# Kernel optimization log

Measured on AMD Instinct MI355X. Metric: run time of the kernel, lower is better.

The kernel has to match this reference:

```python
import jax, jax.numpy as jnp
import numpy as np

N_NODES = 50000
N_EDGES = 800000
IN_CH = 128
EDGE_DIM = 32
H1, H2, H3, OUT = 128, 64, 32, 1


def _linear_params(key, fan_in, fan_out, bias=True):
    k1, k2 = jax.random.split(key)
    scale = 1.0 / np.sqrt(fan_in)
    W = jax.random.uniform(k1, (fan_in, fan_out), jnp.float32, -scale, scale)
    if bias:
        b = jax.random.uniform(k2, (fan_out,), jnp.float32, -scale, scale)
        return W, b
    return W


def setup_inputs() -> dict:
    key = jax.random.key(0)
    ks = jax.random.split(key, 32)
    inp = {
        'x': jax.random.normal(ks[0], (N_NODES, IN_CH), jnp.float32),
        'edge_index': jax.random.randint(ks[1], (2, N_EDGES), 0, N_NODES, jnp.int64),
        'edge_attr': jax.random.normal(ks[2], (N_EDGES, EDGE_DIM), jnp.float32),
    }
    dims = [(IN_CH, H1), (H1, H2), (H2, H3)]
    ki = 3
    for l, (fi, fo) in enumerate(dims, start=1):
        inp[f'Wq{l}'], inp[f'bq{l}'] = _linear_params(ks[ki], fi, fo); ki += 1
        inp[f'Wk{l}'], inp[f'bk{l}'] = _linear_params(ks[ki], fi, fo); ki += 1
        inp[f'Wv{l}'], inp[f'bv{l}'] = _linear_params(ks[ki], fi, fo); ki += 1
        inp[f'We{l}'] = _linear_params(ks[ki], EDGE_DIM, fo, bias=False); ki += 1
        inp[f'Ws{l}'], inp[f'bs{l}'] = _linear_params(ks[ki], fi, fo); ki += 1
    inp['Wc'], inp['bc'] = _linear_params(ks[ki], H3, OUT)
    return inp


def _tconv(x, src, dst, edge_attr, Wq, bq, Wk, bk, Wv, bv, We, Ws, bs):
    # TransformerConv, heads=1: edge-conditioned attention with segment softmax over dst
    q = x @ Wq + bq                      # [N, d]
    k = x @ Wk + bk                      # [N, d]
    v = x @ Wv + bv                      # [N, d]
    e = edge_attr @ We                   # [E, d]
    k_e = k[src] + e                     # gather + edge key
    v_e = v[src] + e                     # gather + edge value
    d = q.shape[-1]
    alpha = jnp.sum(q[dst] * k_e, axis=-1) / jnp.sqrt(jnp.asarray(d, x.dtype))  # [E]
    m = jax.ops.segment_max(alpha, dst, num_segments=N_NODES)
    a = jnp.exp(alpha - m[dst])
    s = jax.ops.segment_sum(a, dst, num_segments=N_NODES)
    a = a / s[dst]
    agg = jax.ops.segment_sum(a[:, None] * v_e, dst, num_segments=N_NODES)
    return agg + x @ Ws + bs             # root/skip connection


def reference(x, edge_index, edge_attr,
              Wq1, bq1, Wk1, bk1, Wv1, bv1, We1, Ws1, bs1,
              Wq2, bq2, Wk2, bk2, Wv2, bv2, We2, Ws2, bs2,
              Wq3, bq3, Wk3, bk3, Wv3, bv3, We3, Ws3, bs3,
              Wc, bc):
    src, dst = edge_index[0], edge_index[1]
    h = jax.nn.relu(_tconv(x, src, dst, edge_attr, Wq1, bq1, Wk1, bk1, Wv1, bv1, We1, Ws1, bs1))
    h = jax.nn.relu(_tconv(h, src, dst, edge_attr, Wq2, bq2, Wk2, bk2, Wv2, bv2, We2, Ws2, bs2))
    h = jax.nn.relu(_tconv(h, src, dst, edge_attr, Wq3, bq3, Wk3, bk3, Wv3, bv3, We3, Ws3, bs3))
    return h @ Wc + bc
```

## Files before the change

kernel.cpp:

```cpp
#include <hip/hip_runtime.h>
#include <math.h>

#define N_NODES 50000
#define N_EDGES 800000

typedef __bf16 bf16;
typedef __bf16 bf16x8 __attribute__((ext_vector_type(8)));
typedef float f32x4 __attribute__((ext_vector_type(4)));

__device__ __forceinline__ float bflo(unsigned r) {
  union { unsigned u; float f; } c; c.u = r << 16; return c.f;
}
__device__ __forceinline__ float bfhi(unsigned r) {
  union { unsigned u; float f; } c; c.u = r & 0xffff0000u; return c.f;
}

__device__ __forceinline__ float dot2bf(unsigned a, unsigned b, float acc) {
#if defined(__has_builtin)
#if __has_builtin(__builtin_amdgcn_fdot2_f32_bf16)
  typedef __bf16 bf16x2 __attribute__((ext_vector_type(2)));
  union { unsigned u; bf16x2 v; } ca, cb;
  ca.u = a; cb.u = b;
  return __builtin_amdgcn_fdot2_f32_bf16(ca.v, cb.v, acc, false);
#else
  return acc + bflo(a) * bflo(b) + bfhi(a) * bfhi(b);
#endif
#else
  return acc + bflo(a) * bflo(b) + bfhi(a) * bfhi(b);
#endif
}

__global__ void k_detect(const int* ei, int* flags) {
  if (threadIdx.x == 0 && blockIdx.x == 0) {
    int is64 = 1;
    for (int i = 0; i < 128; ++i) {
      if (ei[2 * i + 1] != 0) { is64 = 0; break; }
    }
    flags[0] = is64;
  }
}

__device__ __forceinline__ int load_idx(const int* ei, int e, int is64, int which) {
  size_t idx = (size_t)which * N_EDGES + (size_t)e;
  return is64 ? ei[2 * idx] : ei[idx];
}


__global__ void k_zero(int* p, int n) {
  int i = blockIdx.x * blockDim.x + threadIdx.x;
  if (i < n) p[i] = 0;
}

__global__ void k_hist(const int* ei, const int* flags, int* counts) {
  int e = blockIdx.x * blockDim.x + threadIdx.x;
  int is64 = flags[0];
  if (e < N_EDGES) {
    int dst = load_idx(ei, e, is64, 1);
    if (dst >= 0 && dst < N_NODES) atomicAdd(&counts[dst], 1);
  }
}

__global__ void k_scan1(const int* counts, int* row_ptr, int* bsum) {
  __shared__ int buf[1024];
  int t = threadIdx.x;
  int i = blockIdx.x * 1024 + t;
  int v = (i < N_NODES) ? counts[i] : 0;
  buf[t] = v;
  __syncthreads();
  for (int off = 1; off < 1024; off <<= 1) {
    int x = (t >= off) ? buf[t - off] : 0;
    __syncthreads();
    buf[t] += x;
    __syncthreads();
  }
  if (i < N_NODES) row_ptr[i] = buf[t] - v;
  if (t == 1023) bsum[blockIdx.x] = buf[1023];
}

__global__ void k_scan2(int* bsum, int* row_ptr) {
  constexpr int NB = (N_NODES + 1023) / 1024;
  int t = threadIdx.x;
  int v = (t < NB) ? bsum[t] : 0;
  int inc = v;
#pragma unroll
  for (int off = 1; off < 64; off <<= 1) {
    int x = __shfl_up(inc, off, 64);
    if (t >= off) inc += x;
  }
  if (t < NB) bsum[t] = inc - v;
  if (t == 63) row_ptr[N_NODES] = inc;
}

__global__ void k_scan3(const int* bsum, int* row_ptr, int* cursor) {
  int i = blockIdx.x * 1024 + threadIdx.x;
  if (i < N_NODES) {
    int r = row_ptr[i] + bsum[blockIdx.x];
    row_ptr[i] = r;
    cursor[i] = r;
  }
}

__global__ void k_scatter(const int* ei, const int* flags, int* cursor,
                          int* csr_src, int* csr_eid) {
  int e = blockIdx.x * blockDim.x + threadIdx.x;
  int is64 = flags[0];
  if (e < N_EDGES) {
    int src = load_idx(ei, e, is64, 0);
    int dst = load_idx(ei, e, is64, 1);
    if (dst >= 0 && dst < N_NODES && src >= 0 && src < N_NODES) {
      int pos = atomicAdd(&cursor[dst], 1);
      if (pos >= 0 && pos < N_EDGES) {
        csr_src[pos] = src;
        csr_eid[pos] = e;
      }
    }
  }
}


__global__ void k_eaperm(const float* __restrict__ ea, const int* __restrict__ csr_eid,
                         bf16* __restrict__ ea_bf) {
  int idx = blockIdx.x * blockDim.x + threadIdx.x;
  if (idx >= N_EDGES * 16) return;
  int p = idx >> 4, jj = idx & 15;
  int eid = csr_eid[p];
  float2 t = *(const float2*)(ea + (size_t)eid * 32 + 2 * jj);
  union { bf16 b[2]; unsigned u; } c;
  c.b[0] = (bf16)t.x; c.b[1] = (bf16)t.y;
  *(unsigned*)(ea_bf + (size_t)p * 32 + 2 * jj) = c.u;
}


#define DBLK 256
#define NDB ((N_NODES + DBLK - 1) / DBLK)

__global__ void k_dhist(const int* __restrict__ counts, int* __restrict__ btot) {
  __shared__ int lh[64];
  int t = threadIdx.x;
  if (t < 64) lh[t] = 0;
  __syncthreads();
  int n = blockIdx.x * DBLK + t;
  if (n < N_NODES) atomicAdd(&lh[min(counts[n], 63)], 1);
  __syncthreads();
  if (t < 64 && lh[t] > 0) atomicAdd(&btot[t], lh[t]);
}

__global__ void k_dbase(const int* __restrict__ btot, int* __restrict__ dcursor) {
  int t = threadIdx.x;
  int v = btot[t];
  int inc = v;
#pragma unroll
  for (int off = 1; off < 64; off <<= 1) {
    int x = __shfl_up(inc, off, 64);
    if (t >= off) inc += x;
  }
  dcursor[t] = inc - v;
}

__global__ void k_dscatter(const int* __restrict__ counts, int* __restrict__ dcursor,
                           int* __restrict__ node_perm) {
  __shared__ int lh[64];
  __shared__ int lbase[64];
  int t = threadIdx.x;
  if (t < 64) lh[t] = 0;
  __syncthreads();
  int n = blockIdx.x * DBLK + t;
  int b = 0, lrank = 0;
  bool valid = (n < N_NODES);
  if (valid) {
    b = min(counts[n], 63);
    lrank = atomicAdd(&lh[b], 1);
  }
  __syncthreads();
  if (t < 64) {
    int c = lh[t];
    lbase[t] = (c > 0) ? atomicAdd(&dcursor[t], c) : 0;
  }
  __syncthreads();
  if (valid) node_perm[lbase[b] + lrank] = n;
}


template <int FI, int FO>
__global__ void k_prep(const float* __restrict__ Wq, const float* __restrict__ bq,
                       const float* __restrict__ Wk, const float* __restrict__ bk,
                       const float* __restrict__ Wv, const float* __restrict__ bv,
                       const float* __restrict__ We,
                       const float* __restrict__ Ws, const float* __restrict__ bs,
                       bf16* __restrict__ Wt, float* __restrict__ bias) {
  int n = blockIdx.x;
  int k = threadIdx.x;
  if (n < 4 * FO) {
    int sel = n / FO, c = n - sel * FO;
    const float* W = sel == 0 ? Wq : sel == 1 ? Wk : sel == 2 ? Wv : Ws;
    Wt[(size_t)n * FI + k] = (bf16)W[(size_t)k * FO + c];
    if (k == 0) bias[n] = (sel == 0 ? bq : sel == 1 ? bk : sel == 2 ? bv : bs)[c];
  } else {
    int j = n - 4 * FO;
    float acc = 0.f;
    for (int c = 0; c < FO; ++c) acc += Wq[(size_t)k * FO + c] * We[(size_t)j * FO + c];
    Wt[(size_t)n * FI + k] = (bf16)acc;
    if (k == 0) {
      float b = 0.f;
      for (int c = 0; c < FO; ++c) b += bq[c] * We[(size_t)j * FO + c];
      bias[n] = b;
    }
  }
}


template <int K, int FO, bool AF32>
__global__ __launch_bounds__(256) void k_gemm_mfma(const void* __restrict__ A,
                                                   const bf16* __restrict__ Wt,
                                                   const float* __restrict__ bias,
                                                   bf16* __restrict__ feat) {
  constexpr int CPL = FO / 16;
  constexpr int NT = 4 * FO + 32;
  int lane = threadIdx.x & 63;
  int wave = threadIdx.x >> 6;
  int m0 = blockIdx.y * 64 + wave * 16;
  if (m0 >= N_NODES) return;
  int c0 = blockIdx.x * 64;
  int half = lane & 15;
  int quad = lane >> 4;
  f32x4 acc[4] = {};
#pragma unroll
  for (int kb = 0; kb < K; kb += 32) {
    size_t aoff = (size_t)(m0 + half) * K + kb + quad * 8;
    bf16x8 a;
    if constexpr (AF32) {
      const float* Af = (const float*)A;
      f32x4 lo = *(const f32x4*)(Af + aoff);
      f32x4 hi = *(const f32x4*)(Af + aoff + 4);
#pragma unroll
      for (int j = 0; j < 4; ++j) { a[j] = (bf16)lo[j]; a[4 + j] = (bf16)hi[j]; }
    } else {
      a = *(const bf16x8*)((const bf16*)A + aoff);
    }
#pragma unroll
    for (int f = 0; f < 4; ++f) {
      int cb = c0 + f * 16;
      if (cb < NT) {
        bf16x8 b = *(const bf16x8*)(Wt + (size_t)(cb + half) * K + kb + quad * 8);
        acc[f] = __builtin_amdgcn_mfma_f32_16x16x32_bf16(a, b, acc[f], 0, 0, 0);
      }
    }
  }
#pragma unroll
  for (int f = 0; f < 4; ++f) {
    int cb = c0 + f * 16;
    if (cb < NT) {
      int col = cb + half;
      int pos;
      if (col < 4 * FO) {
        int sel = col / FO, c = col - sel * FO;
        if (sel == 0) pos = c;
        else if (sel == 3) pos = 3 * FO + c;
        else {
          int g = c / CPL, o = c - g * CPL;
          pos = FO + g * 2 * CPL + (sel == 2 ? CPL : 0) + o;
        }
      } else {
        pos = col;
      }
      float bv = bias[col];
#pragma unroll
      for (int r = 0; r < 4; ++r) {
        int row = m0 + quad * 4 + r;
        feat[(size_t)row * NT + pos] = (bf16)(acc[f][r] + bv);
      }
    }
  }
}


template <int FO, bool FINAL, bool PERM>
__global__ __launch_bounds__(256) void k_edge(const bf16* __restrict__ feat,
                                              const float* __restrict__ ea,
                                              const bf16* __restrict__ ea_bf,
                                              const int* __restrict__ row_ptr,
                                              const int* __restrict__ csr_src,
                                              const int* __restrict__ csr_eid,
                                              const int* __restrict__ node_perm,
                                              const float* __restrict__ We,
                                              bf16* __restrict__ h_out,
                                              const float* __restrict__ Wc,
                                              const float* __restrict__ bc,
                                              float* __restrict__ out) {
  constexpr int FTOT = 4 * FO + 32;
  constexpr int CPL = FO / 16;
  constexpr int NU = CPL / 2;
  int lane16 = threadIdx.x & 15;
  int gid = blockIdx.x * 16 + (threadIdx.x >> 4);
  int node = node_perm[N_NODES - 1 - gid];
  int cbase = CPL * lane16;
  const bf16* fq = feat + (size_t)node * FTOT;

  unsigned qr[NU];
  {
    const unsigned* qp = (const unsigned*)(fq + cbase);
    if constexpr (NU == 4) { uint4 t = *(const uint4*)qp; qr[0]=t.x; qr[1]=t.y; qr[2]=t.z; qr[3]=t.w; }
    else if constexpr (NU == 2) { uint2 t = *(const uint2*)qp; qr[0]=t.x; qr[1]=t.y; }
    else { qr[0] = *qp; }
  }
  float qe0, qe1;
  { unsigned r = *(const unsigned*)(fq + 4 * FO + 2 * lane16); qe0 = bflo(r); qe1 = bfhi(r); }

  float m = -INFINITY, ssum = 0.f, wacc0 = 0.f, wacc1 = 0.f;
  float vacc[CPL];
#pragma unroll
  for (int i = 0; i < CPL; ++i) vacc[i] = 0.f;

  int start = row_ptr[node], end = row_ptr[node + 1];
  const float scaleA = 1.0f / sqrtf((float)FO);

  auto loadkv = [&](int src, unsigned* kv) {
    const unsigned* base = (const unsigned*)(feat + (size_t)src * FTOT + FO) + CPL * lane16;
    if constexpr (CPL == 8) {
      uint4 a = *(const uint4*)base; uint4 b = *(const uint4*)(base + 4);
      kv[0]=a.x; kv[1]=a.y; kv[2]=a.z; kv[3]=a.w; kv[4]=b.x; kv[5]=b.y; kv[6]=b.z; kv[7]=b.w;
    } else if constexpr (CPL == 4) {
      uint4 a = *(const uint4*)base;
      kv[0]=a.x; kv[1]=a.y; kv[2]=a.z; kv[3]=a.w;
    } else {
      uint2 a = *(const uint2*)base;
      kv[0]=a.x; kv[1]=a.y;
    }
  };

  auto loadea = [&](int p, float& e0, float& e1) {
    if constexpr (PERM) {
      unsigned r = *(const unsigned*)(ea_bf + (size_t)p * 32 + 2 * lane16);
      e0 = bflo(r); e1 = bfhi(r);
    } else {
      int eid = csr_eid[p];
      float2 t = *(const float2*)(ea + (size_t)eid * 32 + 2 * lane16);
      e0 = t.x; e1 = t.y;
    }
  };

  auto update = [&](const unsigned* kv, float e0, float e1) {
    float part = qe0 * e0 + qe1 * e1;
#pragma unroll
    for (int u = 0; u < NU; ++u) part = dot2bf(kv[u], qr[u], part);
#pragma unroll
    for (int off = 1; off < 16; off <<= 1) part += __shfl_xor(part, off, 64);
    float alpha = part * scaleA;
    float mnew = fmaxf(m, alpha);
    float sc = __expf(m - mnew);
    float w = __expf(alpha - mnew);
    ssum = ssum * sc + w;
#pragma unroll
    for (int u = 0; u < NU; ++u) {
      float a = bflo(kv[NU + u]), b = bfhi(kv[NU + u]);
      vacc[2*u]   = vacc[2*u]   * sc + w * a;
      vacc[2*u+1] = vacc[2*u+1] * sc + w * b;
    }
    wacc0 = wacc0 * sc + w * e0;
    wacc1 = wacc1 * sc + w * e1;
    m = mnew;
  };

  int p = start;
  for (; p + 4 <= end; p += 4) {
    int s[4];
#pragma unroll
    for (int u = 0; u < 4; ++u) s[u] = csr_src[p + u];
    unsigned kv[4][8];
#pragma unroll
    for (int u = 0; u < 4; ++u) loadkv(s[u], kv[u]);
    float e0[4], e1[4];
#pragma unroll
    for (int u = 0; u < 4; ++u) loadea(p + u, e0[u], e1[u]);
#pragma unroll
    for (int u = 0; u < 4; ++u) update(kv[u], e0[u], e1[u]);
  }
  for (; p < end; ++p) {
    unsigned kv0[8];
    loadkv(csr_src[p], kv0);
    float e0, e1;
    loadea(p, e0, e1);
    update(kv0, e0, e1);
  }

  float inv = (ssum > 0.f) ? 1.0f / ssum : 0.f;
  float agg[CPL];
#pragma unroll
  for (int i = 0; i < CPL; ++i) agg[i] = vacc[i];
#pragma unroll
  for (int jh = 0; jh < 16; ++jh) {
    float w0 = __shfl(wacc0, jh, 16);
    float w1 = __shfl(wacc1, jh, 16);
    const float* r0 = We + (size_t)(2 * jh) * FO + cbase;
    const float* r1 = We + (size_t)(2 * jh + 1) * FO + cbase;
#pragma unroll
    for (int i = 0; i < CPL; ++i) agg[i] += w0 * r0[i] + w1 * r1[i];
  }
  float hv[CPL];
#pragma unroll
  for (int i = 0; i < CPL; ++i) {
    float s = (float)fq[3 * FO + cbase + i];
    hv[i] = fmaxf(agg[i] * inv + s, 0.f);
  }
  if constexpr (!FINAL) {
    unsigned o[NU];
#pragma unroll
    for (int u = 0; u < NU; ++u) {
      union { bf16 b[2]; unsigned u32; } c;
      c.b[0] = (bf16)hv[2*u]; c.b[1] = (bf16)hv[2*u+1];
      o[u] = c.u32;
    }
    unsigned* dst = (unsigned*)(h_out + (size_t)node * FO + cbase);
    if constexpr (NU == 4) { uint4 t; t.x=o[0]; t.y=o[1]; t.z=o[2]; t.w=o[3]; *(uint4*)dst = t; }
    else if constexpr (NU == 2) { uint2 t; t.x=o[0]; t.y=o[1]; *(uint2*)dst = t; }
    else { *dst = o[0]; }
  } else {
    float part2 = 0.f;
#pragma unroll
    for (int i = 0; i < CPL; ++i) part2 += hv[i] * Wc[cbase + i];
#pragma unroll
    for (int off = 1; off < 16; off <<= 1) part2 += __shfl_xor(part2, off, 64);
    if (lane16 == 0) out[node] = part2 + bc[0];
  }
}


extern "C" void kernel_launch(void* const* d_in, const int* in_sizes, int n_in,
                              void* d_out, int out_size, void* d_ws, size_t ws_size,
                              hipStream_t stream) {
  (void)in_sizes; (void)n_in; (void)out_size;
  const float* x = (const float*)d_in[0];
  const int* ei = (const int*)d_in[1];
  const float* ea = (const float*)d_in[2];
  const float *Wq1 = (const float*)d_in[3], *bq1 = (const float*)d_in[4];
  const float *Wk1 = (const float*)d_in[5], *bk1 = (const float*)d_in[6];
  const float *Wv1 = (const float*)d_in[7], *bv1 = (const float*)d_in[8];
  const float *We1 = (const float*)d_in[9];
  const float *Ws1 = (const float*)d_in[10], *bs1 = (const float*)d_in[11];
  const float *Wq2 = (const float*)d_in[12], *bq2 = (const float*)d_in[13];
  const float *Wk2 = (const float*)d_in[14], *bk2 = (const float*)d_in[15];
  const float *Wv2 = (const float*)d_in[16], *bv2 = (const float*)d_in[17];
  const float *We2 = (const float*)d_in[18];
  const float *Ws2 = (const float*)d_in[19], *bs2 = (const float*)d_in[20];
  const float *Wq3 = (const float*)d_in[21], *bq3 = (const float*)d_in[22];
  const float *Wk3 = (const float*)d_in[23], *bk3 = (const float*)d_in[24];
  const float *Wv3 = (const float*)d_in[25], *bv3 = (const float*)d_in[26];
  const float *We3 = (const float*)d_in[27];
  const float *Ws3 = (const float*)d_in[28], *bs3 = (const float*)d_in[29];
  const float *Wc = (const float*)d_in[30], *bc = (const float*)d_in[31];

  char* ws = (char*)d_ws;
  size_t off = 0;
  auto alloc = [&](size_t bytes) -> void* {
    void* p = ws + off;
    off = (off + bytes + 255) & ~(size_t)255;
    return p;
  };
  bf16* h        = (bf16*)alloc((size_t)N_NODES * 128 * 2);
  int* counts    = (int*)alloc((N_NODES + 1) * 4);
  int* row_ptr   = (int*)alloc((N_NODES + 1) * 4);
  int* cursor    = (int*)alloc((N_NODES + 1) * 4);
  int* csr_src   = (int*)alloc((size_t)N_EDGES * 4);
  int* csr_eid   = (int*)alloc((size_t)N_EDGES * 4);
  int* flags     = (int*)alloc(256);
  bf16* Wt       = (bf16*)alloc(544 * 128 * 2);
  float* bias    = (float*)alloc(544 * 4);
  bf16* feat     = (bf16*)alloc((size_t)N_NODES * 544 * 2);
  int* bsum      = (int*)alloc(64 * 4);
  int* dcount    = (int*)alloc(64 * 4);
  int* dcursor   = (int*)alloc(64 * 4);
  int* node_perm = (int*)alloc((size_t)N_NODES * 4);
  size_t off_base = off;
  bf16* ea_bf    = (bf16*)alloc((size_t)N_EDGES * 32 * 2);
  bool use_perm = (ws_size == 0) || (off <= ws_size);
  (void)off_base;

  constexpr int NB = (N_NODES + 1023) / 1024;

  k_detect<<<1, 1, 0, stream>>>(ei, flags);
  k_zero<<<(N_NODES + 256) / 256, 256, 0, stream>>>(counts, N_NODES + 1);
  k_zero<<<1, 64, 0, stream>>>(dcount, 64);
  k_hist<<<(N_EDGES + 255) / 256, 256, 0, stream>>>(ei, flags, counts);
  k_scan1<<<NB, 1024, 0, stream>>>(counts, row_ptr, bsum);
  k_scan2<<<1, 64, 0, stream>>>(bsum, row_ptr);
  k_scan3<<<NB, 1024, 0, stream>>>(bsum, row_ptr, cursor);
  k_dhist<<<NDB, DBLK, 0, stream>>>(counts, dcount);
  k_dbase<<<1, 64, 0, stream>>>(dcount, dcursor);
  k_dscatter<<<NDB, DBLK, 0, stream>>>(counts, dcursor, node_perm);
  k_scatter<<<(N_EDGES + 255) / 256, 256, 0, stream>>>(ei, flags, cursor, csr_src, csr_eid);
  if (use_perm) {
    k_eaperm<<<(N_EDGES * 16 + 255) / 256, 256, 0, stream>>>(ea, csr_eid, ea_bf);
  }

  k_prep<128, 128><<<544, 128, 0, stream>>>(Wq1, bq1, Wk1, bk1, Wv1, bv1, We1, Ws1, bs1,
                                            Wt, bias);
  {
    dim3 g((544 + 63) / 64, (N_NODES + 63) / 64);
    k_gemm_mfma<128, 128, true><<<g, 256, 0, stream>>>(x, Wt, bias, feat);
  }
  if (use_perm)
    k_edge<128, false, true><<<N_NODES / 16, 256, 0, stream>>>(feat, ea, ea_bf, row_ptr,
                                                               csr_src, csr_eid, node_perm,
                                                               We1, h, nullptr, nullptr,
                                                               nullptr);
  else
    k_edge<128, false, false><<<N_NODES / 16, 256, 0, stream>>>(feat, ea, ea_bf, row_ptr,
                                                                csr_src, csr_eid, node_perm,
                                                                We1, h, nullptr, nullptr,
                                                                nullptr);

  k_prep<128, 64><<<288, 128, 0, stream>>>(Wq2, bq2, Wk2, bk2, Wv2, bv2, We2, Ws2, bs2,
                                           Wt, bias);
  {
    dim3 g((288 + 63) / 64, (N_NODES + 63) / 64);
    k_gemm_mfma<128, 64, false><<<g, 256, 0, stream>>>(h, Wt, bias, feat);
  }
  if (use_perm)
    k_edge<64, false, true><<<N_NODES / 16, 256, 0, stream>>>(feat, ea, ea_bf, row_ptr,
                                                              csr_src, csr_eid, node_perm,
                                                              We2, h, nullptr, nullptr,
                                                              nullptr);
  else
    k_edge<64, false, false><<<N_NODES / 16, 256, 0, stream>>>(feat, ea, ea_bf, row_ptr,
                                                               csr_src, csr_eid, node_perm,
                                                               We2, h, nullptr, nullptr,
                                                               nullptr);

  k_prep<64, 32><<<160, 64, 0, stream>>>(Wq3, bq3, Wk3, bk3, Wv3, bv3, We3, Ws3, bs3,
                                         Wt, bias);
  {
    dim3 g((160 + 63) / 64, (N_NODES + 63) / 64);
    k_gemm_mfma<64, 32, false><<<g, 256, 0, stream>>>(h, Wt, bias, feat);
  }
  if (use_perm)
    k_edge<32, true, true><<<N_NODES / 16, 256, 0, stream>>>(feat, ea, ea_bf, row_ptr,
                                                             csr_src, csr_eid, node_perm,
                                                             We3, nullptr, Wc, bc,
                                                             (float*)d_out);
  else
    k_edge<32, true, false><<<N_NODES / 16, 256, 0, stream>>>(feat, ea, ea_bf, row_ptr,
                                                              csr_src, csr_eid, node_perm,
                                                              We3, nullptr, Wc, bc,
                                                              (float*)d_out);
}
```

Measured before the change: 671.6 us.

## Restructure node GEMM: load A once per block, permute weights in prep, pack stores

```diff
diff --git a/kernel.cpp b/kernel.cpp
--- a/kernel.cpp
+++ b/kernel.cpp
@@ -188,86 +188,93 @@
                        const float* __restrict__ We,
                        const float* __restrict__ Ws, const float* __restrict__ bs,
                        bf16* __restrict__ Wt, float* __restrict__ bias) {
+  constexpr int CPL = FO / 16;
   int n = blockIdx.x;
   int k = threadIdx.x;
+  int pos;
+  if (n < 4 * FO) {
+    int sel = n / FO, c = n - sel * FO;
+    if (sel == 0) pos = c;
+    else if (sel == 3) pos = 3 * FO + c;
+    else {
+      int g = c / CPL, o = c - g * CPL;
+      pos = FO + g * 2 * CPL + (sel == 2 ? CPL : 0) + o;
+    }
+  } else {
+    pos = n;
+  }
   if (n < 4 * FO) {
     int sel = n / FO, c = n - sel * FO;
     const float* W = sel == 0 ? Wq : sel == 1 ? Wk : sel == 2 ? Wv : Ws;
-    Wt[(size_t)n * FI + k] = (bf16)W[(size_t)k * FO + c];
-    if (k == 0) bias[n] = (sel == 0 ? bq : sel == 1 ? bk : sel == 2 ? bv : bs)[c];
+    Wt[(size_t)pos * FI + k] = (bf16)W[(size_t)k * FO + c];
+    if (k == 0) bias[pos] = (sel == 0 ? bq : sel == 1 ? bk : sel == 2 ? bv : bs)[c];
   } else {
     int j = n - 4 * FO;
     float acc = 0.f;
     for (int c = 0; c < FO; ++c) acc += Wq[(size_t)k * FO + c] * We[(size_t)j * FO + c];
-    Wt[(size_t)n * FI + k] = (bf16)acc;
+    Wt[(size_t)pos * FI + k] = (bf16)acc;
     if (k == 0) {
       float b = 0.f;
       for (int c = 0; c < FO; ++c) b += bq[c] * We[(size_t)j * FO + c];
-      bias[n] = b;
-    }
-  }
-}
-
-
-template <int K, int FO, bool AF32>
+      bias[pos] = b;
+    }
+  }
+}
+
+
+template <int K, int NT, bool AF32>
 __global__ __launch_bounds__(256) void k_gemm_mfma(const void* __restrict__ A,
                                                    const bf16* __restrict__ Wt,
                                                    const float* __restrict__ bias,
                                                    bf16* __restrict__ feat) {
-  constexpr int CPL = FO / 16;
-  constexpr int NT = 4 * FO + 32;
+  constexpr int NKB = K / 32;
+  constexpr int NCH = (NT + 63) / 64;
   int lane = threadIdx.x & 63;
   int wave = threadIdx.x >> 6;
-  int m0 = blockIdx.y * 64 + wave * 16;
+  int m0 = blockIdx.x * 64 + wave * 16;
   if (m0 >= N_NODES) return;
-  int c0 = blockIdx.x * 64;
   int half = lane & 15;
   int quad = lane >> 4;
-  f32x4 acc[4] = {};
-#pragma unroll
-  for (int kb = 0; kb < K; kb += 32) {
-    size_t aoff = (size_t)(m0 + half) * K + kb + quad * 8;
-    bf16x8 a;
+
+  bf16x8 afr[NKB];
+#pragma unroll
+  for (int kb = 0; kb < NKB; ++kb) {
+    size_t aoff = (size_t)(m0 + half) * K + kb * 32 + quad * 8;
     if constexpr (AF32) {
       const float* Af = (const float*)A;
       f32x4 lo = *(const f32x4*)(Af + aoff);
       f32x4 hi = *(const f32x4*)(Af + aoff + 4);
 #pragma unroll
-      for (int j = 0; j < 4; ++j) { a[j] = (bf16)lo[j]; a[4 + j] = (bf16)hi[j]; }
+      for (int j = 0; j < 4; ++j) { afr[kb][j] = (bf16)lo[j]; afr[kb][4 + j] = (bf16)hi[j]; }
     } else {
-      a = *(const bf16x8*)((const bf16*)A + aoff);
+      afr[kb] = *(const bf16x8*)((const bf16*)A + aoff);
+    }
+  }
+
+  for (int ch = 0; ch < NCH; ++ch) {
+    int c0 = ch * 64;
+    f32x4 acc[4] = {};
+#pragma unroll
+    for (int kb = 0; kb < NKB; ++kb) {
+#pragma unroll
+      for (int f = 0; f < 4; ++f) {
+        int cb = c0 + f * 16;
+        if (cb < NT) {
+          bf16x8 b = *(const bf16x8*)(Wt + (size_t)(cb + half) * K + kb * 32 + quad * 8);
+          acc[f] = __builtin_amdgcn_mfma_f32_16x16x32_bf16(b, afr[kb], acc[f], 0, 0, 0);
+        }
+      }
     }
 #pragma unroll
     for (int f = 0; f < 4; ++f) {
       int cb = c0 + f * 16;
       if (cb < NT) {
-        bf16x8 b = *(const bf16x8*)(Wt + (size_t)(cb + half) * K + kb + quad * 8);
-        acc[f] = __builtin_amdgcn_mfma_f32_16x16x32_bf16(a, b, acc[f], 0, 0, 0);
-      }
-    }
-  }
-#pragma unroll
-  for (int f = 0; f < 4; ++f) {
-    int cb = c0 + f * 16;
-    if (cb < NT) {
-      int col = cb + half;
-      int pos;
-      if (col < 4 * FO) {
-        int sel = col / FO, c = col - sel * FO;
-        if (sel == 0) pos = c;
-        else if (sel == 3) pos = 3 * FO + c;
-        else {
-          int g = c / CPL, o = c - g * CPL;
-          pos = FO + g * 2 * CPL + (sel == 2 ? CPL : 0) + o;
-        }
-      } else {
-        pos = col;
-      }
-      float bv = bias[col];
-#pragma unroll
-      for (int r = 0; r < 4; ++r) {
-        int row = m0 + quad * 4 + r;
-        feat[(size_t)row * NT + pos] = (bf16)(acc[f][r] + bv);
+        int fcol = cb + quad * 4;
+        f32x4 bv = *(const f32x4*)(bias + fcol);
+        union { bf16 b[4]; uint2 u; } pk;
+#pragma unroll
+        for (int r = 0; r < 4; ++r) pk.b[r] = (bf16)(acc[f][r] + bv[r]);
+        *(uint2*)(feat + (size_t)(m0 + half) * NT + fcol) = pk.u;
       }
     }
   }
@@ -470,12 +477,11 @@
   int* dcount    = (int*)alloc(64 * 4);
   int* dcursor   = (int*)alloc(64 * 4);
   int* node_perm = (int*)alloc((size_t)N_NODES * 4);
-  size_t off_base = off;
   bf16* ea_bf    = (bf16*)alloc((size_t)N_EDGES * 32 * 2);
   bool use_perm = (ws_size == 0) || (off <= ws_size);
-  (void)off_base;
 
   constexpr int NB = (N_NODES + 1023) / 1024;
+  constexpr int GB = (N_NODES + 63) / 64;
 
   k_detect<<<1, 1, 0, stream>>>(ei, flags);
   k_zero<<<(N_NODES + 256) / 256, 256, 0, stream>>>(counts, N_NODES + 1);
@@ -494,10 +500,7 @@
 
   k_prep<128, 128><<<544, 128, 0, stream>>>(Wq1, bq1, Wk1, bk1, Wv1, bv1, We1, Ws1, bs1,
                                             Wt, bias);
-  {
-    dim3 g((544 + 63) / 64, (N_NODES + 63) / 64);
-    k_gemm_mfma<128, 128, true><<<g, 256, 0, stream>>>(x, Wt, bias, feat);
-  }
+  k_gemm_mfma<128, 544, true><<<GB, 256, 0, stream>>>(x, Wt, bias, feat);
   if (use_perm)
     k_edge<128, false, true><<<N_NODES / 16, 256, 0, stream>>>(feat, ea, ea_bf, row_ptr,
                                                                csr_src, csr_eid, node_perm,
@@ -511,10 +514,7 @@
 
   k_prep<128, 64><<<288, 128, 0, stream>>>(Wq2, bq2, Wk2, bk2, Wv2, bv2, We2, Ws2, bs2,
                                            Wt, bias);
-  {
-    dim3 g((288 + 63) / 64, (N_NODES + 63) / 64);
-    k_gemm_mfma<128, 64, false><<<g, 256, 0, stream>>>(h, Wt, bias, feat);
-  }
+  k_gemm_mfma<128, 288, false><<<GB, 256, 0, stream>>>(h, Wt, bias, feat);
   if (use_perm)
     k_edge<64, false, true><<<N_NODES / 16, 256, 0, stream>>>(feat, ea, ea_bf, row_ptr,
                                                               csr_src, csr_eid, node_perm,
@@ -528,10 +528,7 @@
 
   k_prep<64, 32><<<160, 64, 0, stream>>>(Wq3, bq3, Wk3, bk3, Wv3, bv3, We3, Ws3, bs3,
                                          Wt, bias);
-  {
-    dim3 g((160 + 63) / 64, (N_NODES + 63) / 64);
-    k_gemm_mfma<64, 32, false><<<g, 256, 0, stream>>>(h, Wt, bias, feat);
-  }
+  k_gemm_mfma<64, 160, false><<<GB, 256, 0, stream>>>(h, Wt, bias, feat);
   if (use_perm)
     k_edge<32, true, true><<<N_NODES / 16, 256, 0, stream>>>(feat, ea, ea_bf, row_ptr,
                                                              csr_src, csr_eid, node_perm,
```

Result: faster. 654.0 us (-2.6%).
